# Kernel tuning notes

Measured on AMD Instinct MI355X. Metric: run time of the kernel, lower is better.

Reference implementation:

```python
import jax, jax.numpy as jnp
import numpy as np
import math

N_HEADS = 16
D_MODEL = 1024
D_K = D_MODEL // N_HEADS
NEG_INF = -1e9
LN_EPS = 1e-5


def setup_inputs() -> dict:
    key = jax.random.key(0)
    ks = jax.random.split(key, 10)
    B, S = 8, 1024
    x = jax.random.normal(ks[0], (B, S, D_MODEL), dtype=jnp.float32)
    mask = jnp.ones((B, S, 1), dtype=jnp.float32)
    s = 1.0 / math.sqrt(D_MODEL)
    # per-head Linear weights, torch layout [out, in] stacked over heads
    wq = jax.random.uniform(ks[1], (N_HEADS, D_K, D_MODEL), jnp.float32, -s, s)
    bq = jax.random.uniform(ks[2], (N_HEADS, D_K), jnp.float32, -s, s)
    wk = jax.random.uniform(ks[3], (N_HEADS, D_K, D_MODEL), jnp.float32, -s, s)
    bk = jax.random.uniform(ks[4], (N_HEADS, D_K), jnp.float32, -s, s)
    wv = jax.random.uniform(ks[5], (N_HEADS, D_K, D_MODEL), jnp.float32, -s, s)
    bv = jax.random.uniform(ks[6], (N_HEADS, D_K), jnp.float32, -s, s)
    w_out = jax.random.uniform(ks[7], (D_MODEL, D_MODEL), jnp.float32, -s, s)
    b_out = jax.random.uniform(ks[8], (D_MODEL,), jnp.float32, -s, s)
    return {"x": x, "mask": mask, "wq": wq, "bq": bq, "wk": wk, "bk": bk,
            "wv": wv, "bv": bv, "w_out": w_out, "b_out": b_out}


def _masked_softmax(scores, mask2d, axis):
    # mask2d: [B,S,S] broadcast over heads; zero entries get -1e9 before softmax
    masked = jnp.where(mask2d[:, None, :, :] > 0, scores, NEG_INF)
    return jax.nn.softmax(masked, axis=axis)


def reference(x, mask, wq, bq, wk, bk, wv, bv, w_out, b_out):
    B, S, D = x.shape
    # layer_norm over last dim, no affine params (F.layer_norm defaults)
    mu = jnp.mean(x, axis=-1, keepdims=True)
    var = jnp.var(x, axis=-1, keepdims=True)
    xn = (x - mu) * jax.lax.rsqrt(var + LN_EPS)
    # batched per-head projections: [B,H,S,d_k]
    q = jnp.einsum('bsd,hkd->bhsk', xn, wq) + bq[None, :, None, :]
    k = jnp.einsum('bsd,hkd->bhsk', xn, wk) + bk[None, :, None, :]
    v = jnp.einsum('bsd,hkd->bhsk', xn, wv) + bv[None, :, None, :]
    scores = jnp.einsum('bhsk,bhtk->bhst', q, k) / math.sqrt(D_K)
    mask2d = jnp.einsum('bsi,bti->bst', mask, mask)  # [B,S,S]
    # double masked softmax: first over query dim (torch dim=1), then key dim (dim=2)
    attn = _masked_softmax(scores, mask2d, axis=2)
    attn = _masked_softmax(attn, mask2d, axis=3)
    heads = jnp.einsum('bhst,bhtk->bshk', attn, v)  # [B,S,H,d_v]
    heads = heads.reshape(B, S, D)
    return heads @ w_out.T + b_out + x
```

## Files before the change

kernel.cpp:

```cpp
#include <hip/hip_runtime.h>


typedef unsigned short ushort_t;
typedef unsigned short us4 __attribute__((ext_vector_type(4)));
typedef unsigned short us8 __attribute__((ext_vector_type(8)));
typedef __bf16 bf16x8 __attribute__((ext_vector_type(8)));
typedef float f32x4 __attribute__((ext_vector_type(4)));

#define QSCALE 0.18033688011112042f
#define LOG2E 1.4426950408889634f
#define MNEG (-1.0e9f)
#define EXP2(x) __builtin_amdgcn_exp2f(x)

__device__ __forceinline__ ushort_t f2bf(float f) {
    unsigned int u = __float_as_uint(f);
    return (ushort_t)((u + 0x7fffu + ((u >> 16) & 1u)) >> 16);
}

__device__ __forceinline__ int xcd_remap() {
    int nwg = gridDim.x * gridDim.y * gridDim.z;
    int o = blockIdx.x + gridDim.x * (blockIdx.y + gridDim.y * blockIdx.z);
    int q = nwg >> 3, r = nwg & 7;
    int xcd = o & 7, i = o >> 3;
    return (xcd < r ? xcd * (q + 1) : r * (q + 1) + (xcd - r) * q) + i;
}

#define GLDS(gp, lp)                                                        \
    __builtin_amdgcn_global_load_lds(                                       \
        (const __attribute__((address_space(1))) unsigned int*)(gp),        \
        (__attribute__((address_space(3))) unsigned int*)(lp), 16, 0, 0)

#define MFMA(a, b, c) __builtin_amdgcn_mfma_f32_16x16x32_bf16((a), (b), (c), 0, 0, 0)

__global__ __launch_bounds__(256) void ln_kernel(const float* __restrict__ x,
                                                 ushort_t* __restrict__ xn) {
    int row = blockIdx.x, tid = threadIdx.x;
    float4 v = ((const float4*)(x + (size_t)row * 1024))[tid];
    float s = v.x + v.y + v.z + v.w;
    __shared__ float red[8];
    for (int o = 32; o > 0; o >>= 1) s += __shfl_down(s, o);
    int wave = tid >> 6, lane = tid & 63;
    if (lane == 0) red[wave] = s;
    __syncthreads();
    float mu = (red[0] + red[1] + red[2] + red[3]) * (1.0f / 1024.0f);
    float d0 = v.x - mu, d1 = v.y - mu, d2 = v.z - mu, d3 = v.w - mu;
    float q = d0 * d0 + d1 * d1 + d2 * d2 + d3 * d3;
    for (int o = 32; o > 0; o >>= 1) q += __shfl_down(q, o);
    if (lane == 0) red[wave + 4] = q;
    __syncthreads();
    float var = (red[4] + red[5] + red[6] + red[7]) * (1.0f / 1024.0f);
    float rs = rsqrtf(var + 1e-5f);
    us4 ov;
    ov[0] = f2bf(d0 * rs); ov[1] = f2bf(d1 * rs);
    ov[2] = f2bf(d2 * rs); ov[3] = f2bf(d3 * rs);
    ((us4*)(xn + (size_t)row * 1024))[tid] = ov;
}

__global__ __launch_bounds__(256) void wconv(const float* __restrict__ src,
                                             ushort_t* __restrict__ dst) {
    size_t i = ((size_t)blockIdx.x * 256 + threadIdx.x) * 4;
    float4 f = *(const float4*)(src + i);
    us4 o;
    o[0] = f2bf(f.x); o[1] = f2bf(f.y); o[2] = f2bf(f.z); o[3] = f2bf(f.w);
    *(us4*)(dst + i) = o;
}

__global__ __launch_bounds__(256) void tailcopy(const us8* __restrict__ src,
                                                us8* __restrict__ dst) {
    size_t i = (size_t)blockIdx.x * 256 + threadIdx.x;
    dst[i] = src[i];
}

template <int BMODE, int OMODE>
__global__ __launch_bounds__(256) void gemm_mfma(
    const ushort_t* __restrict__ A, const void* __restrict__ Bq,
    const void* __restrict__ Bk, const void* __restrict__ Bv,
    const float* __restrict__ biasq, const float* __restrict__ biask,
    const float* __restrict__ biasv, ushort_t* __restrict__ oq,
    ushort_t* __restrict__ ok, ushort_t* __restrict__ ovt,
    float* __restrict__ ofp, const float* __restrict__ resx, int batched,
    int r0base, int aoff) {
    __shared__ ushort_t As[2][128 * 32] __attribute__((aligned(16)));
    __shared__ ushort_t Bs[2][128 * 32] __attribute__((aligned(16)));
    int tid = threadIdx.x, w = tid >> 6, lane = tid & 63;
    int quad = lane >> 4, l15 = lane & 15;
    int wm = w & 1, wn = w >> 1;
    int csw = (quad ^ ((l15 >> 1) & 3)) * 8;
    int wg = xcd_remap();
    int gxz = gridDim.x * gridDim.z;
    int wy = wg / gxz, wt = wg % gxz;
    int n0 = (wt % gridDim.x) * 128;
    int r0 = r0base + wy * 128;
    int wsel = wt / gridDim.x;
    const void* Bp = (wsel == 0) ? Bq : (wsel == 1) ? Bk : Bv;
    const float* biasp = (wsel == 0) ? biasq : (wsel == 1) ? biask : biasv;
    const float qscale = (OMODE == 0 && wsel == 0) ? QSCALE : 1.0f;

    auto stage = [&](int buf, int k0) {
#pragma unroll
        for (int ii = 0; ii < 2; ii++) {
            int li = (w * 2 + ii) * 64 + lane;
            int row = li >> 2, kc = li & 3;
            int sk = kc ^ ((row >> 1) & 3);
            GLDS(A + (size_t)(r0 + row - aoff) * 1024 + k0 + sk * 8,
                 &As[buf][(w * 2 + ii) * 512]);
        }
        if (BMODE == 0) {
#pragma unroll
            for (int ii = 0; ii < 2; ii++) {
                int li = (w * 2 + ii) * 64 + lane;
                int row = li >> 2, kc = li & 3;
                int sk = kc ^ ((row >> 1) & 3);
                GLDS((const ushort_t*)Bp + (size_t)(n0 + row) * 1024 + k0 + sk * 8,
                     &Bs[buf][(w * 2 + ii) * 512]);
            }
        } else {
            int row = tid >> 1, half = tid & 1;
            int sw = (row >> 1) & 3;
            const float* gb =
                (const float*)Bp + (size_t)(n0 + row) * 1024 + k0 + half * 16;
            float4 f0 = *(const float4*)gb;
            float4 f1 = *(const float4*)(gb + 4);
            float4 f2 = *(const float4*)(gb + 8);
            float4 f3 = *(const float4*)(gb + 12);
            us8 p0, p1;
            p0[0] = f2bf(f0.x); p0[1] = f2bf(f0.y); p0[2] = f2bf(f0.z); p0[3] = f2bf(f0.w);
            p0[4] = f2bf(f1.x); p0[5] = f2bf(f1.y); p0[6] = f2bf(f1.z); p0[7] = f2bf(f1.w);
            p1[0] = f2bf(f2.x); p1[1] = f2bf(f2.y); p1[2] = f2bf(f2.z); p1[3] = f2bf(f2.w);
            p1[4] = f2bf(f3.x); p1[5] = f2bf(f3.y); p1[6] = f2bf(f3.z); p1[7] = f2bf(f3.w);
            *(us8*)&Bs[buf][row * 32 + ((half * 2) ^ sw) * 8] = p0;
            *(us8*)&Bs[buf][row * 32 + ((half * 2 + 1) ^ sw) * 8] = p1;
        }
    };

    f32x4 acc[4][4];
    stage(0, 0);
#pragma unroll
    for (int i = 0; i < 4; i++)
#pragma unroll
        for (int j = 0; j < 4; j++) acc[i][j] = (f32x4){0.f, 0.f, 0.f, 0.f};
    __syncthreads();

    int cur = 0;
    for (int k0 = 0; k0 < 1024; k0 += 32) {
        if (k0 + 32 < 1024) stage(cur ^ 1, k0 + 32);
        bf16x8 a[4], b[4];
#pragma unroll
        for (int i = 0; i < 4; i++)
            a[i] = *(const bf16x8*)&As[cur][(wm * 64 + i * 16 + l15) * 32 + csw];
#pragma unroll
        for (int j = 0; j < 4; j++)
            b[j] = *(const bf16x8*)&Bs[cur][(wn * 64 + j * 16 + l15) * 32 + csw];
#pragma unroll
        for (int i = 0; i < 4; i++)
#pragma unroll
            for (int j = 0; j < 4; j++) acc[i][j] = MFMA(a[i], b[j], acc[i][j]);
        __syncthreads();
        cur ^= 1;
    }
#pragma unroll
    for (int j = 0; j < 4; j++) {
        int n = n0 + wn * 64 + j * 16 + l15;
        float bj = biasp[n];
        if (OMODE == 0) {
            int h = n >> 6, kk = n & 63;
#pragma unroll
            for (int i = 0; i < 4; i++) {
#pragma unroll
                for (int v = 0; v < 4; v++) {
                    int r = r0 + wm * 64 + i * 16 + quad * 4 + v;
                    int bb = batched ? (r >> 10) : 0;
                    int s = r & 1023;
                    ushort_t val = f2bf((acc[i][j][v] + bj) * qscale);
                    if (wsel < 2) {
                        ushort_t* op = (wsel == 0) ? oq : ok;
                        op[((size_t)(bb * 16 + h) * 1024 + s) * 64 + kk] = val;
                    } else {
                        ovt[((size_t)(bb * 16 + h) * 64 + kk) * 1024 + s] = val;
                    }
                }
            }
        } else {
#pragma unroll
            for (int i = 0; i < 4; i++) {
#pragma unroll
                for (int v = 0; v < 4; v++) {
                    int r = r0 + wm * 64 + i * 16 + quad * 4 + v;
                    size_t idx = (size_t)r * 1024 + n;
                    ofp[idx] = acc[i][j][v] + bj + resx[idx];
                }
            }
        }
    }
}

__global__ __launch_bounds__(256) void colstats_mfma(
    const ushort_t* __restrict__ qb, const ushort_t* __restrict__ kb,
    const float* __restrict__ mask, int moff, float* __restrict__ colsum) {
    __shared__ ushort_t Ks[4096] __attribute__((aligned(16)));
    __shared__ ushort_t Qs[4096] __attribute__((aligned(16)));
    __shared__ float mk[64], mq[64], red[4][64];
    int tid = threadIdx.x, w = tid >> 6, lane = tid & 63;
    int quad = lane >> 4, l15 = lane & 15;
    int csw = (quad ^ ((l15 >> 1) & 3)) * 8;
    int wg = xcd_remap();
    int by = wg / gridDim.x;
    int t0 = (wg % gridDim.x) * 64;
    size_t qoff = (size_t)by * 65536;
    int coff = by * 1024;
    int mb = moff + (by >> 4) * 1024;
#pragma unroll
    for (int ii = 0; ii < 2; ii++) {
        int qq = w * 2 + ii, half = qq >> 2, sub = qq & 3;
        int li = sub * 64 + lane, row = li >> 2, seg = li & 3;
        int sk = seg ^ ((row >> 1) & 3);
        GLDS(kb + qoff + (size_t)(t0 + row) * 64 + half * 32 + sk * 8,
             &Ks[half * 2048 + sub * 512]);
    }
    if (tid < 64) mk[tid] = mask[mb + t0 + tid];
    __syncthreads();
    bf16x8 kf0[4], kf1[4];
#pragma unroll
    for (int j = 0; j < 4; j++) {
        kf0[j] = *(const bf16x8*)&Ks[(j * 16 + l15) * 32 + csw];
        kf1[j] = *(const bf16x8*)&Ks[2048 + (j * 16 + l15) * 32 + csw];
    }
    float amk[4];
#pragma unroll
    for (int j = 0; j < 4; j++) amk[j] = (mk[j * 16 + l15] > 0.f) ? 0.f : MNEG;
    float colacc[4] = {0.f, 0.f, 0.f, 0.f};
    for (int s0 = 0; s0 < 1024; s0 += 64) {
        __syncthreads();
#pragma unroll
        for (int ii = 0; ii < 2; ii++) {
            int qq = w * 2 + ii, half = qq >> 2, sub = qq & 3;
            int li = sub * 64 + lane, row = li >> 2, seg = li & 3;
            int sk = seg ^ ((row >> 1) & 3);
            GLDS(qb + qoff + (size_t)(s0 + row) * 64 + half * 32 + sk * 8,
                 &Qs[half * 2048 + sub * 512]);
        }
        if (tid < 64) mq[tid] = mask[mb + s0 + tid];
        __syncthreads();
        float amq[4];
#pragma unroll
        for (int v = 0; v < 4; v++)
            amq[v] = (mq[w * 16 + quad * 4 + v] > 0.f) ? 0.f : MNEG;
        bf16x8 a0 = *(const bf16x8*)&Qs[(w * 16 + l15) * 32 + csw];
        bf16x8 a1 = *(const bf16x8*)&Qs[2048 + (w * 16 + l15) * 32 + csw];
#pragma unroll
        for (int j = 0; j < 4; j++) {
            f32x4 sc = (f32x4){0.f, 0.f, 0.f, 0.f};
            sc = MFMA(a0, kf0[j], sc);
            sc = MFMA(a1, kf1[j], sc);
#pragma unroll
            for (int v = 0; v < 4; v++)
                colacc[j] += EXP2(sc[v] + amq[v] + amk[j]);
        }
    }
#pragma unroll
    for (int j = 0; j < 4; j++) {
        float vv = colacc[j];
        vv += __shfl_down(vv, 32);
        vv += __shfl_down(vv, 16);
        if (quad == 0) red[w][j * 16 + l15] = vv;
    }
    __syncthreads();
    if (tid < 64)
        colsum[coff + t0 + tid] = red[0][tid] + red[1][tid] + red[2][tid] + red[3][tid];
}

__global__ __launch_bounds__(256) void pv_mfma(
    const ushort_t* __restrict__ qb, const ushort_t* __restrict__ kb,
    const ushort_t* __restrict__ vtb, const float* __restrict__ mask, int moff,
    const float* __restrict__ colsum, ushort_t* __restrict__ H, int hbase) {
    __shared__ ushort_t Qs[4096] __attribute__((aligned(16)));
    __shared__ ushort_t Ks[4096] __attribute__((aligned(16)));
    __shared__ ushort_t Vt[4096] __attribute__((aligned(16)));
    __shared__ ushort_t E[64 * 72] __attribute__((aligned(16)));
    __shared__ float mk[64], mq[64], ics[64];
    int tid = threadIdx.x, w = tid >> 6, lane = tid & 63;
    int quad = lane >> 4, l15 = lane & 15;
    int csw = (quad ^ ((l15 >> 1) & 3)) * 8;
    int wg = xcd_remap();
    int by = wg / gridDim.x;
    int s0 = (wg % gridDim.x) * 64;
    size_t qoff = (size_t)by * 65536;
    int coff = by * 1024;
    int mb = moff + (by >> 4) * 1024;
    int h = by & 15;
#pragma unroll
    for (int ii = 0; ii < 2; ii++) {
        int qq = w * 2 + ii, half = qq >> 2, sub = qq & 3;
        int li = sub * 64 + lane, row = li >> 2, seg = li & 3;
        int sk = seg ^ ((row >> 1) & 3);
        GLDS(qb + qoff + (size_t)(s0 + row) * 64 + half * 32 + sk * 8,
             &Qs[half * 2048 + sub * 512]);
    }
    if (tid < 64) mq[tid] = mask[mb + s0 + tid];
    __syncthreads();
    bf16x8 a0 = *(const bf16x8*)&Qs[(w * 16 + l15) * 32 + csw];
    bf16x8 a1 = *(const bf16x8*)&Qs[2048 + (w * 16 + l15) * 32 + csw];
    float amq[4];
#pragma unroll
    for (int v = 0; v < 4; v++)
        amq[v] = (mq[w * 16 + quad * 4 + v] > 0.f) ? 0.f : MNEG;
    bf16x8 ones;
#pragma unroll
    for (int e = 0; e < 8; e++) ones[e] = (__bf16)1.0f;
    f32x4 acc_o[4], acc_rs = (f32x4){0.f, 0.f, 0.f, 0.f};
#pragma unroll
    for (int j = 0; j < 4; j++) acc_o[j] = (f32x4){0.f, 0.f, 0.f, 0.f};
    for (int t0 = 0; t0 < 1024; t0 += 64) {
        __syncthreads();
#pragma unroll
        for (int ii = 0; ii < 2; ii++) {
            int qq = w * 2 + ii, half = qq >> 2, sub = qq & 3;
            int li = sub * 64 + lane, row = li >> 2, seg = li & 3;
            int sk = seg ^ ((row >> 1) & 3);
            GLDS(kb + qoff + (size_t)(t0 + row) * 64 + half * 32 + sk * 8,
                 &Ks[half * 2048 + sub * 512]);
            GLDS(vtb + qoff + (size_t)row * 1024 + t0 + half * 32 + sk * 8,
                 &Vt[half * 2048 + sub * 512]);
        }
        if (tid < 64) {
            mk[tid] = mask[mb + t0 + tid];
            float cs = colsum[coff + t0 + tid];
            ics[tid] = (cs > 0.f) ? LOG2E / cs : 0.f;
        }
        __syncthreads();
#pragma unroll
        for (int j = 0; j < 4; j++) {
            bf16x8 b0 = *(const bf16x8*)&Ks[(j * 16 + l15) * 32 + csw];
            bf16x8 b1 = *(const bf16x8*)&Ks[2048 + (j * 16 + l15) * 32 + csw];
            f32x4 sc = (f32x4){0.f, 0.f, 0.f, 0.f};
            sc = MFMA(a0, b0, sc);
            sc = MFMA(a1, b1, sc);
            int tcol = j * 16 + l15;
            float icv = ics[tcol];
            float aj = (mk[tcol] > 0.f) ? 0.f : MNEG;
#pragma unroll
            for (int v = 0; v < 4; v++) {
                float e1 = EXP2(sc[v]);
                float e2 = EXP2(fmaf(e1, icv, amq[v] + aj));
                int sl = w * 16 + quad * 4 + v;
                E[sl * 72 + tcol] = (ushort_t)(__float_as_uint(e2) >> 16);
            }
        }
        bf16x8 ea0 = *(const bf16x8*)&E[(w * 16 + l15) * 72 + quad * 8];
        bf16x8 ea1 = *(const bf16x8*)&E[(w * 16 + l15) * 72 + 32 + quad * 8];
#pragma unroll
        for (int j = 0; j < 4; j++) {
            bf16x8 b0 = *(const bf16x8*)&Vt[(j * 16 + l15) * 32 + csw];
            bf16x8 b1 = *(const bf16x8*)&Vt[2048 + (j * 16 + l15) * 32 + csw];
            acc_o[j] = MFMA(ea0, b0, acc_o[j]);
            acc_o[j] = MFMA(ea1, b1, acc_o[j]);
        }
        acc_rs = MFMA(ea0, ones, acc_rs);
        acc_rs = MFMA(ea1, ones, acc_rs);
    }
#pragma unroll
    for (int v = 0; v < 4; v++) {
        int sl = w * 16 + quad * 4 + v;
        int hr = hbase + (by >> 4) * 1024 + s0 + sl;
        ushort_t* hp = H + (size_t)hr * 1024;
        float inv = 1.0f / fmaxf(acc_rs[v], 1e-30f);
#pragma unroll
        for (int j = 0; j < 4; j++)
            hp[h * 64 + j * 16 + l15] = f2bf(acc_o[j][v] * inv);
    }
}

extern "C" void kernel_launch(void* const* d_in, const int* in_sizes, int n_in,
                              void* d_out, int out_size, void* d_ws, size_t ws_size,
                              hipStream_t stream) {
    const float* x     = (const float*)d_in[0];
    const float* mask  = (const float*)d_in[1];
    const float* wq    = (const float*)d_in[2];
    const float* bq    = (const float*)d_in[3];
    const float* wk    = (const float*)d_in[4];
    const float* bk    = (const float*)d_in[5];
    const float* wv    = (const float*)d_in[6];
    const float* bv    = (const float*)d_in[7];
    const float* w_out = (const float*)d_in[8];
    const float* b_out = (const float*)d_in[9];
    float* outp = (float*)d_out;

    const size_t MB = 1024 * 1024;
    ushort_t* xn = (ushort_t*)d_out;
    ushort_t* H  = (ushort_t*)d_out + 8 * MB;
    char* ws = (char*)d_ws;

    ln_kernel<<<dim3(8192), 256, 0, stream>>>(x, xn);

    if (ws_size >= 58 * MB) {
        ushort_t* qb  = (ushort_t*)ws;
        ushort_t* kb  = (ushort_t*)(ws + 16 * MB);
        ushort_t* vtb = (ushort_t*)(ws + 32 * MB);
        float* csum   = (float*)(ws + 48 * MB);
        ushort_t* wqb = (ushort_t*)(ws + 49 * MB);
        ushort_t* wkb = (ushort_t*)(ws + 51 * MB);
        ushort_t* wvb = (ushort_t*)(ws + 53 * MB);
        ushort_t* wob = (ushort_t*)(ws + 55 * MB);
        float* ofull  = (float*)ws;
        wconv<<<dim3(1024), 256, 0, stream>>>(wq, wqb);
        wconv<<<dim3(1024), 256, 0, stream>>>(wk, wkb);
        wconv<<<dim3(1024), 256, 0, stream>>>(wv, wvb);
        wconv<<<dim3(1024), 256, 0, stream>>>(w_out, wob);
        gemm_mfma<0, 0><<<dim3(8, 64, 3), 256, 0, stream>>>(
            xn, wqb, wkb, wvb, bq, bk, bv, qb, kb, vtb, nullptr, nullptr, 1, 0, 0);
        colstats_mfma<<<dim3(16, 128), 256, 0, stream>>>(qb, kb, mask, 0, csum);
        pv_mfma<<<dim3(16, 128), 256, 0, stream>>>(qb, kb, vtb, mask, 0, csum, H, 0);
        gemm_mfma<0, 1><<<dim3(8, 64), 256, 0, stream>>>(
            H, wob, wob, wob, b_out, b_out, b_out, nullptr, nullptr, nullptr,
            ofull, x, 0, 0, 0);
        hipMemcpyAsync(d_out, ofull, 32 * MB, hipMemcpyDeviceToDevice, stream);
    } else {
        ushort_t* qb  = (ushort_t*)ws;
        ushort_t* kb  = (ushort_t*)(ws + 2 * MB);
        ushort_t* vtb = (ushort_t*)(ws + 4 * MB);
        float* csum   = (float*)(ws + 6 * MB);
        ushort_t* hcopy = (ushort_t*)ws;
        const int casc[6][2] = {{0, 32},   {4096, 16}, {6144, 8},
                                {7168, 4}, {7680, 2},  {7936, 1}};
        for (int g = 0; g < 8; g++) {
            gemm_mfma<1, 0><<<dim3(8, 8, 3), 256, 0, stream>>>(
                xn + (size_t)g * MB, wq, wk, wv, bq, bk, bv, qb, kb, vtb,
                nullptr, nullptr, 0, 0, 0);
            colstats_mfma<<<dim3(16, 16), 256, 0, stream>>>(qb, kb, mask,
                                                            g * 1024, csum);
            pv_mfma<<<dim3(16, 16), 256, 0, stream>>>(qb, kb, vtb, mask,
                                                      g * 1024, csum, H, g * 1024);
        }
        tailcopy<<<dim3(64), 256, 0, stream>>>((const us8*)(H + (size_t)8064 * 1024),
                                               (us8*)hcopy);
        for (int i = 0; i < 6; i++)
            gemm_mfma<1, 1><<<dim3(8, casc[i][1]), 256, 0, stream>>>(
                H, w_out, w_out, w_out, b_out, b_out, b_out, nullptr, nullptr,
                nullptr, outp, x, 0, casc[i][0], 0);
        gemm_mfma<1, 1><<<dim3(8, 1), 256, 0, stream>>>(
            hcopy, w_out, w_out, w_out, b_out, b_out, b_out, nullptr, nullptr,
            nullptr, outp, x, 0, 8064, 8064);
    }
}
```

Measured before the change: 360.0 us.

## Transpose V tile via LDS, merge weight conversions, split output GEMM to halve copy

The four weight-conversion launches are merged into one 2D-grid kernel. The V projection epilogue now stages the tile transposed in shared memory so each thread writes contiguous 16-byte chunks instead of scattered 2-byte stores. The output GEMM is split into two halves: the first writes directly into the output buffer, the second into workspace, so only 16 MB has to be copied back instead of 32 MB. The XCD remapping is also dropped from the attention kernels in favour of plain block indices, which may change L2 locality.

New measurement: 340.3 us. 1.06x faster.

```diff
diff --git a/kernel.cpp b/kernel.cpp
--- a/kernel.cpp
+++ b/kernel.cpp
@@ -56,13 +56,19 @@
     ((us4*)(xn + (size_t)row * 1024))[tid] = ov;
 }
 
-__global__ __launch_bounds__(256) void wconv(const float* __restrict__ src,
-                                             ushort_t* __restrict__ dst) {
+__global__ __launch_bounds__(256) void wconv4(
+    const float* __restrict__ s0, const float* __restrict__ s1,
+    const float* __restrict__ s2, const float* __restrict__ s3,
+    ushort_t* __restrict__ d0, ushort_t* __restrict__ d1,
+    ushort_t* __restrict__ d2, ushort_t* __restrict__ d3) {
+    int sel = blockIdx.y;
+    const float* s = (sel == 0) ? s0 : (sel == 1) ? s1 : (sel == 2) ? s2 : s3;
+    ushort_t* d = (sel == 0) ? d0 : (sel == 1) ? d1 : (sel == 2) ? d2 : d3;
     size_t i = ((size_t)blockIdx.x * 256 + threadIdx.x) * 4;
-    float4 f = *(const float4*)(src + i);
+    float4 f = *(const float4*)(s + i);
     us4 o;
     o[0] = f2bf(f.x); o[1] = f2bf(f.y); o[2] = f2bf(f.z); o[3] = f2bf(f.w);
-    *(us4*)(dst + i) = o;
+    *(us4*)(d + i) = o;
 }
 
 __global__ __launch_bounds__(256) void tailcopy(const us8* __restrict__ src,
@@ -79,9 +85,10 @@
     const float* __restrict__ biasv, ushort_t* __restrict__ oq,
     ushort_t* __restrict__ ok, ushort_t* __restrict__ ovt,
     float* __restrict__ ofp, const float* __restrict__ resx, int batched,
-    int r0base, int aoff) {
-    __shared__ ushort_t As[2][128 * 32] __attribute__((aligned(16)));
-    __shared__ ushort_t Bs[2][128 * 32] __attribute__((aligned(16)));
+    int r0base, int aoff, int osub) {
+    __shared__ ushort_t SMEM[4][128 * 32] __attribute__((aligned(16)));
+#define AS_(b) (SMEM[(b)])
+#define BS_(b) (SMEM[2 + (b)])
     int tid = threadIdx.x, w = tid >> 6, lane = tid & 63;
     int quad = lane >> 4, l15 = lane & 15;
     int wm = w & 1, wn = w >> 1;
@@ -103,7 +110,7 @@
             int row = li >> 2, kc = li & 3;
             int sk = kc ^ ((row >> 1) & 3);
             GLDS(A + (size_t)(r0 + row - aoff) * 1024 + k0 + sk * 8,
-                 &As[buf][(w * 2 + ii) * 512]);
+                 &AS_(buf)[(w * 2 + ii) * 512]);
         }
         if (BMODE == 0) {
 #pragma unroll
@@ -112,7 +119,7 @@
                 int row = li >> 2, kc = li & 3;
                 int sk = kc ^ ((row >> 1) & 3);
                 GLDS((const ushort_t*)Bp + (size_t)(n0 + row) * 1024 + k0 + sk * 8,
-                     &Bs[buf][(w * 2 + ii) * 512]);
+                     &BS_(buf)[(w * 2 + ii) * 512]);
             }
         } else {
             int row = tid >> 1, half = tid & 1;
@@ -128,8 +135,8 @@
             p0[4] = f2bf(f1.x); p0[5] = f2bf(f1.y); p0[6] = f2bf(f1.z); p0[7] = f2bf(f1.w);
             p1[0] = f2bf(f2.x); p1[1] = f2bf(f2.y); p1[2] = f2bf(f2.z); p1[3] = f2bf(f2.w);
             p1[4] = f2bf(f3.x); p1[5] = f2bf(f3.y); p1[6] = f2bf(f3.z); p1[7] = f2bf(f3.w);
-            *(us8*)&Bs[buf][row * 32 + ((half * 2) ^ sw) * 8] = p0;
-            *(us8*)&Bs[buf][row * 32 + ((half * 2 + 1) ^ sw) * 8] = p1;
+            *(us8*)&BS_(buf)[row * 32 + ((half * 2) ^ sw) * 8] = p0;
+            *(us8*)&BS_(buf)[row * 32 + ((half * 2 + 1) ^ sw) * 8] = p1;
         }
     };
 
@@ -147,10 +154,10 @@
         bf16x8 a[4], b[4];
 #pragma unroll
         for (int i = 0; i < 4; i++)
-            a[i] = *(const bf16x8*)&As[cur][(wm * 64 + i * 16 + l15) * 32 + csw];
+            a[i] = *(const bf16x8*)&AS_(cur)[(wm * 64 + i * 16 + l15) * 32 + csw];
 #pragma unroll
         for (int j = 0; j < 4; j++)
-            b[j] = *(const bf16x8*)&Bs[cur][(wn * 64 + j * 16 + l15) * 32 + csw];
+            b[j] = *(const bf16x8*)&BS_(cur)[(wn * 64 + j * 16 + l15) * 32 + csw];
 #pragma unroll
         for (int i = 0; i < 4; i++)
 #pragma unroll
@@ -158,40 +165,67 @@
         __syncthreads();
         cur ^= 1;
     }
-#pragma unroll
-    for (int j = 0; j < 4; j++) {
-        int n = n0 + wn * 64 + j * 16 + l15;
-        float bj = biasp[n];
-        if (OMODE == 0) {
-            int h = n >> 6, kk = n & 63;
-#pragma unroll
-            for (int i = 0; i < 4; i++) {
+    if (OMODE == 0 && wsel == 2) {
+        ushort_t* TP = &SMEM[0][0];
+#pragma unroll
+        for (int j = 0; j < 4; j++) {
+            int nl = wn * 64 + j * 16 + l15;
+            float bj = biasp[n0 + nl];
+#pragma unroll
+            for (int i = 0; i < 4; i++)
 #pragma unroll
                 for (int v = 0; v < 4; v++) {
-                    int r = r0 + wm * 64 + i * 16 + quad * 4 + v;
-                    int bb = batched ? (r >> 10) : 0;
-                    int s = r & 1023;
-                    ushort_t val = f2bf((acc[i][j][v] + bj) * qscale);
-                    if (wsel < 2) {
+                    int rl = wm * 64 + i * 16 + quad * 4 + v;
+                    TP[nl * 128 + (rl ^ ((nl & 15) << 3))] =
+                        f2bf(acc[i][j][v] + bj);
+                }
+        }
+        __syncthreads();
+        int row = tid >> 1, half = tid & 1;
+        int n = n0 + row, hh = n >> 6, kk = n & 63;
+        int bb = batched ? (r0 >> 10) : 0;
+        int sbase = (r0 & 1023) + half * 64;
+        ushort_t* gp = ovt + ((size_t)(bb * 16 + hh) * 64 + kk) * 1024 + sbase;
+#pragma unroll
+        for (int c = 0; c < 8; c++) {
+            us8 vv = *(const us8*)&TP[row * 128 +
+                                      ((half * 64 + c * 8) ^ ((row & 15) << 3))];
+            *(us8*)(gp + c * 8) = vv;
+        }
+    } else {
+#pragma unroll
+        for (int j = 0; j < 4; j++) {
+            int n = n0 + wn * 64 + j * 16 + l15;
+            float bj = biasp[n];
+            if (OMODE == 0) {
+                int h = n >> 6, kk = n & 63;
+#pragma unroll
+                for (int i = 0; i < 4; i++) {
+#pragma unroll
+                    for (int v = 0; v < 4; v++) {
+                        int r = r0 + wm * 64 + i * 16 + quad * 4 + v;
+                        int bb = batched ? (r >> 10) : 0;
+                        int s = r & 1023;
+                        ushort_t val = f2bf((acc[i][j][v] + bj) * qscale);
                         ushort_t* op = (wsel == 0) ? oq : ok;
                         op[((size_t)(bb * 16 + h) * 1024 + s) * 64 + kk] = val;
-                    } else {
-                        ovt[((size_t)(bb * 16 + h) * 64 + kk) * 1024 + s] = val;
+                    }
+                }
+            } else {
+#pragma unroll
+                for (int i = 0; i < 4; i++) {
+#pragma unroll
+                    for (int v = 0; v < 4; v++) {
+                        int r = r0 + wm * 64 + i * 16 + quad * 4 + v;
+                        ofp[(size_t)(r - osub) * 1024 + n] =
+                            acc[i][j][v] + bj + resx[(size_t)r * 1024 + n];
                     }
                 }
             }
-        } else {
-#pragma unroll
-            for (int i = 0; i < 4; i++) {
-#pragma unroll
-                for (int v = 0; v < 4; v++) {
-                    int r = r0 + wm * 64 + i * 16 + quad * 4 + v;
-                    size_t idx = (size_t)r * 1024 + n;
-                    ofp[idx] = acc[i][j][v] + bj + resx[idx];
-                }
-            }
-        }
-    }
+        }
+    }
+#undef AS_
+#undef BS_
 }
 
 __global__ __launch_bounds__(256) void colstats_mfma(
@@ -203,12 +237,11 @@
     int tid = threadIdx.x, w = tid >> 6, lane = tid & 63;
     int quad = lane >> 4, l15 = lane & 15;
     int csw = (quad ^ ((l15 >> 1) & 3)) * 8;
-    int wg = xcd_remap();
-    int by = wg / gridDim.x;
-    int t0 = (wg % gridDim.x) * 64;
+    int by = blockIdx.y;
     size_t qoff = (size_t)by * 65536;
     int coff = by * 1024;
     int mb = moff + (by >> 4) * 1024;
+    int t0 = blockIdx.x * 64;
 #pragma unroll
     for (int ii = 0; ii < 2; ii++) {
         int qq = w * 2 + ii, half = qq >> 2, sub = qq & 3;
@@ -281,13 +314,12 @@
     int tid = threadIdx.x, w = tid >> 6, lane = tid & 63;
     int quad = lane >> 4, l15 = lane & 15;
     int csw = (quad ^ ((l15 >> 1) & 3)) * 8;
-    int wg = xcd_remap();
-    int by = wg / gridDim.x;
-    int s0 = (wg % gridDim.x) * 64;
+    int by = blockIdx.y;
     size_t qoff = (size_t)by * 65536;
     int coff = by * 1024;
     int mb = moff + (by >> 4) * 1024;
     int h = by & 15;
+    int s0 = blockIdx.x * 64;
 #pragma unroll
     for (int ii = 0; ii < 2; ii++) {
         int qq = w * 2 + ii, half = qq >> 2, sub = qq & 3;
@@ -401,19 +433,22 @@
         ushort_t* wkb = (ushort_t*)(ws + 51 * MB);
         ushort_t* wvb = (ushort_t*)(ws + 53 * MB);
         ushort_t* wob = (ushort_t*)(ws + 55 * MB);
-        float* ofull  = (float*)ws;
-        wconv<<<dim3(1024), 256, 0, stream>>>(wq, wqb);
-        wconv<<<dim3(1024), 256, 0, stream>>>(wk, wkb);
-        wconv<<<dim3(1024), 256, 0, stream>>>(wv, wvb);
-        wconv<<<dim3(1024), 256, 0, stream>>>(w_out, wob);
+        float* ohi    = (float*)ws;
+        wconv4<<<dim3(1024, 4), 256, 0, stream>>>(wq, wk, wv, w_out,
+                                                  wqb, wkb, wvb, wob);
         gemm_mfma<0, 0><<<dim3(8, 64, 3), 256, 0, stream>>>(
-            xn, wqb, wkb, wvb, bq, bk, bv, qb, kb, vtb, nullptr, nullptr, 1, 0, 0);
+            xn, wqb, wkb, wvb, bq, bk, bv, qb, kb, vtb, nullptr, nullptr, 1,
+            0, 0, 0);
         colstats_mfma<<<dim3(16, 128), 256, 0, stream>>>(qb, kb, mask, 0, csum);
         pv_mfma<<<dim3(16, 128), 256, 0, stream>>>(qb, kb, vtb, mask, 0, csum, H, 0);
-        gemm_mfma<0, 1><<<dim3(8, 64), 256, 0, stream>>>(
+        gemm_mfma<0, 1><<<dim3(8, 32), 256, 0, stream>>>(
             H, wob, wob, wob, b_out, b_out, b_out, nullptr, nullptr, nullptr,
-            ofull, x, 0, 0, 0);
-        hipMemcpyAsync(d_out, ofull, 32 * MB, hipMemcpyDeviceToDevice, stream);
+            (float*)d_out, x, 0, 0, 0, 0);
+        gemm_mfma<0, 1><<<dim3(8, 32), 256, 0, stream>>>(
+            H, wob, wob, wob, b_out, b_out, b_out, nullptr, nullptr, nullptr,
+            ohi, x, 0, 4096, 0, 4096);
+        hipMemcpyAsync((char*)d_out + 16 * MB, ws, 16 * MB,
+                       hipMemcpyDeviceToDevice, stream);
     } else {
         ushort_t* qb  = (ushort_t*)ws;
         ushort_t* kb  = (ushort_t*)(ws + 2 * MB);
@@ -425,7 +460,7 @@
         for (int g = 0; g < 8; g++) {
             gemm_mfma<1, 0><<<dim3(8, 8, 3), 256, 0, stream>>>(
                 xn + (size_t)g * MB, wq, wk, wv, bq, bk, bv, qb, kb, vtb,
-                nullptr, nullptr, 0, 0, 0);
+                nullptr, nullptr, 0, 0, 0, 0);
             colstats_mfma<<<dim3(16, 16), 256, 0, stream>>>(qb, kb, mask,
                                                             g * 1024, csum);
             pv_mfma<<<dim3(16, 16), 256, 0, stream>>>(qb, kb, vtb, mask,
@@ -436,9 +471,9 @@
         for (int i = 0; i < 6; i++)
             gemm_mfma<1, 1><<<dim3(8, casc[i][1]), 256, 0, stream>>>(
                 H, w_out, w_out, w_out, b_out, b_out, b_out, nullptr, nullptr,
-                nullptr, outp, x, 0, casc[i][0], 0);
+                nullptr, outp, x, 0, casc[i][0], 0, 0);
         gemm_mfma<1, 1><<<dim3(8, 1), 256, 0, stream>>>(
             hcopy, w_out, w_out, w_out, b_out, b_out, b_out, nullptr, nullptr,
-            nullptr, outp, x, 0, 8064, 8064);
-    }
-}
+            nullptr, outp, x, 0, 8064, 8064, 0);
+    }
+}
```
